# Performance work log

Hardware: AMD Instinct MI355X
Metric: run time of the kernel (lower is better)

Reference implementation:

```python
import jax, jax.numpy as jnp
import numpy as np

B, T, C, H = 2, 2048, 1024, 16
HS = C // H  # head_size = 64
EPS = 1e-5


def _ln(x, g, b):
    m = jnp.mean(x, axis=-1, keepdims=True)
    v = jnp.mean(jnp.square(x - m), axis=-1, keepdims=True)
    return (x - m) * jax.lax.rsqrt(v + EPS) * g + b


def setup_inputs() -> dict:
    key = jax.random.key(0)
    ks = jax.random.split(key, 16)
    s = lambda k, shape, fan: jax.random.normal(k, shape, jnp.float32) * (fan ** -0.5)
    return {
        "x": jax.random.normal(ks[0], (B, T, C), jnp.float32),
        "Wq": s(ks[1], (H, C, HS), C), "bq": jnp.zeros((H, HS), jnp.float32),
        "Wk": s(ks[2], (H, C, HS), C), "bk": jnp.zeros((H, HS), jnp.float32),
        "Wv": s(ks[3], (H, C, HS), C), "bv": jnp.zeros((H, HS), jnp.float32),
        "Wo": s(ks[4], (C, C), C), "bo": jnp.zeros((C,), jnp.float32),
        "g1": jnp.ones((C,), jnp.float32), "b1": jnp.zeros((C,), jnp.float32),
        "g2": jnp.ones((C,), jnp.float32), "b2": jnp.zeros((C,), jnp.float32),
        "W1": s(ks[5], (C, C), C), "bf1": jnp.zeros((C,), jnp.float32),
        "W2": s(ks[6], (C, C), C), "bf2": jnp.zeros((C,), jnp.float32),
    }


def _block(x, Wq, bq, Wk, bk, Wv, bv, Wo, bo, g1, b1, g2, b2, W1, bf1, W2, bf2):
    h = _ln(x, g1, b1)
    # per-head projections, batched over heads: (B,T,C) x (H,C,HS) -> (B,H,T,HS)
    q = jnp.einsum('btc,hcd->bhtd', h, Wq) + bq[None, :, None, :]
    k = jnp.einsum('btc,hcd->bhtd', h, Wk) + bk[None, :, None, :]
    v = jnp.einsum('btc,hcd->bhtd', h, Wv) + bv[None, :, None, :]
    w = jnp.einsum('bhqd,bhkd->bhqk', q, k) * (HS ** -0.5)
    causal = jnp.tril(jnp.ones((T, T), bool))  # tril[q,k]==0 -> -inf
    w = jnp.where(causal[None, None], w, -jnp.inf)
    # FAITHFUL quirk: original uses F.softmax(w, dim=1) on (B,T,T),
    # i.e. normalization over the QUERY axis (axis=2 of bhqk).
    w = jax.nn.softmax(w, axis=2)
    att = jnp.einsum('bhqk,bhkd->bhqd', w, v)
    att = att.transpose(0, 2, 1, 3).reshape(x.shape[0], x.shape[1], -1)  # concat heads
    x = x + att @ Wo + bo
    h2 = _ln(x, g2, b2)
    x = x + jax.nn.relu(h2 @ W1 + bf1) @ W2 + bf2
    return x


def reference(x, Wq, bq, Wk, bk, Wv, bv, Wo, bo, g1, b1, g2, b2, W1, bf1, W2, bf2):
    return _block(x, Wq, bq, Wk, bk, Wv, bv, Wo, bo, g1, b1, g2, b2, W1, bf1, W2, bf2)
```

## Files before the change

### kernel.cpp

```cpp
#include <hip/hip_runtime.h>
#include <hip/hip_bf16.h>
#include <math.h>


#define B_   2
#define T_   2048
#define C_   1024
#define H_   16
#define HS_  64
#define NROWS 4096
#define C3   3072
#define K1C  0.1803368801111244f

typedef unsigned short ushort_t;
typedef __attribute__((ext_vector_type(8))) short short8;
typedef __attribute__((ext_vector_type(4))) float f32x4;
typedef __attribute__((ext_vector_type(16))) float f32x16;

__device__ __forceinline__ ushort_t f2bf(float f) {
  __hip_bfloat16 h = __float2bfloat16(f);
  ushort_t u; __builtin_memcpy(&u, &h, 2); return u;
}
__device__ __forceinline__ float bf2f(ushort_t u) {
  union { unsigned u; float f; } v; v.u = ((unsigned)u) << 16;
  return v.f;
}
__device__ __forceinline__ unsigned pkhw(float a, float b) {
  unsigned u;
  asm("v_cvt_pk_bf16_f32 %0, %1, %2" : "=v"(u) : "v"(a), "v"(b));
  return u;
}
__device__ __forceinline__ short8 mk8(unsigned a, unsigned b, unsigned c, unsigned d) {
  union { unsigned u[4]; short8 s; } t;
  t.u[0] = a; t.u[1] = b; t.u[2] = c; t.u[3] = d; return t.s;
}
__device__ __forceinline__ void pl32swap(unsigned &a, unsigned &b) {
  asm("v_permlane32_swap_b32 %0, %1" : "+v"(a), "+v"(b));
}
__device__ __forceinline__ f32x4 mfma16(short8 a, short8 b, f32x4 c) {
  return __builtin_amdgcn_mfma_f32_16x16x32_bf16(a, b, c, 0, 0, 0);
}
__device__ __forceinline__ f32x16 mfma32(short8 a, short8 b, f32x16 c) {
  return __builtin_amdgcn_mfma_f32_32x32x16_bf16(a, b, c, 0, 0, 0);
}
typedef const __attribute__((address_space(1))) void g_void;
typedef __attribute__((address_space(3))) void l_void;
__device__ __forceinline__ void gl_lds16(const void* g, void* l) {
  __builtin_amdgcn_global_load_lds((g_void*)g, (l_void*)l, 16, 0, 0);
}

__global__ __launch_bounds__(256) void ln_bf16(
    const float* __restrict__ x, const float* __restrict__ g,
    const float* __restrict__ b, ushort_t* __restrict__ out) {
  int row = blockIdx.x;
  const float* xr = x + (size_t)row * C_;
  int t = threadIdx.x;
  float4 v = ((const float4*)xr)[t];
  float s  = v.x + v.y + v.z + v.w;
  float ss = v.x*v.x + v.y*v.y + v.z*v.z + v.w*v.w;
  #pragma unroll
  for (int off = 32; off > 0; off >>= 1) {
    s  += __shfl_down(s, off);
    ss += __shfl_down(ss, off);
  }
  __shared__ float red[2][4];
  int wid = t >> 6, lane = t & 63;
  if (lane == 0) { red[0][wid] = s; red[1][wid] = ss; }
  __syncthreads();
  if (t == 0) {
    float a = 0, c = 0;
    for (int i = 0; i < 4; i++) { a += red[0][i]; c += red[1][i]; }
    red[0][0] = a; red[1][0] = c;
  }
  __syncthreads();
  float mean = red[0][0] * (1.0f / C_);
  float var  = red[1][0] * (1.0f / C_) - mean * mean;
  float r = rsqrtf(var + 1e-5f);
  float4 gv = ((const float4*)g)[t];
  float4 bv = ((const float4*)b)[t];
  ushort4 o;
  o.x = f2bf((v.x - mean) * r * gv.x + bv.x);
  o.y = f2bf((v.y - mean) * r * gv.y + bv.y);
  o.z = f2bf((v.z - mean) * r * gv.z + bv.z);
  o.w = f2bf((v.w - mean) * r * gv.w + bv.w);
  ((ushort4*)(out + (size_t)row * C_))[t] = o;
}

__global__ __launch_bounds__(256) void prep_weights(
    const float* __restrict__ Wq, const float* __restrict__ Wk,
    const float* __restrict__ Wv, const float* __restrict__ Wo,
    const float* __restrict__ W1, const float* __restrict__ W2,
    const float* __restrict__ bq, const float* __restrict__ bk,
    const float* __restrict__ bv, ushort_t* __restrict__ Wqkvt,
    ushort_t* __restrict__ Wot3, float* __restrict__ bqkv) {
  int bid = blockIdx.x;
  if (bid < 12288) {
    int idx = bid * 256 + threadIdx.x;
    int n = idx >> 10, c = idx & 1023;
    int sel = n >> 10, nn = n & 1023;
    const float* W = (sel == 0) ? Wq : ((sel == 1) ? Wk : Wv);
    Wqkvt[idx] = f2bf(W[((size_t)(nn >> 6) * C_ + c) * HS_ + (nn & 63)]);
  } else if (bid < 24576) {
    int idx = (bid - 12288) * 256 + threadIdx.x;
    int sel = idx >> 20, rem = idx & 1048575;
    int n = rem >> 10, k = rem & 1023;
    const float* W = (sel == 0) ? Wo : ((sel == 1) ? W1 : W2);
    Wot3[idx] = f2bf(W[(size_t)k * C_ + n]);
  } else {
    int i = (bid - 24576) * 256 + threadIdx.x;
    if (i < 3072)
      bqkv[i] = (i < 1024) ? bq[i] : ((i < 2048) ? bk[i - 1024] : bv[i - 2048]);
  }
}

__global__ __launch_bounds__(256) void gemm128q(
    const ushort_t* __restrict__ A, const ushort_t* __restrict__ Bt,
    const float* __restrict__ bias, ushort_t* __restrict__ Cm,
    int M, int N, int K) {
  __shared__ ushort_t As[2][128 * 32];
  __shared__ ushort_t Bs[2][128 * 32];
  int t = threadIdx.x;
  int bid = blockIdx.x;
  int xcd = bid & 7, loc = bid >> 3;
  int mb = (xcd >> 1) * 8 + (loc & 7);
  int nb = (xcd & 1) * 12 + (loc >> 3);
  int m0 = mb * 128, n0 = nb * 128;
  int w = t >> 6, l = t & 63;
  int wr = w >> 1, wc = w & 1;
  int lo = l & 15, hi = l >> 4;
  f32x4 acc[4][4] = {};
  int srow = t >> 2;
  int sslot = (t & 3) ^ ((srow >> 1) & 3);
  const ushort_t* Ag = A  + (size_t)(m0 + srow) * K + sslot * 8;
  const ushort_t* Bg = Bt + (size_t)(n0 + srow) * K + sslot * 8;
  int key = (lo >> 1) & 3;
  int aoff[4], boff[4];
  #pragma unroll
  for (int i = 0; i < 4; i++) {
    aoff[i] = (wr * 64 + i * 16 + lo) * 32 + (hi ^ key) * 8;
    boff[i] = (wc * 64 + i * 16 + lo) * 32 + (hi ^ key) * 8;
  }
  int nkt = K >> 5;
  gl_lds16(Ag,          &As[0][t * 8]);
  gl_lds16(Ag + 64 * K, &As[0][64 * 32 + t * 8]);
  gl_lds16(Bg,          &Bs[0][t * 8]);
  gl_lds16(Bg + 64 * K, &Bs[0][64 * 32 + t * 8]);
  for (int kt = 0; kt < nkt; kt++) {
    int cur = kt & 1;
    if (kt + 1 < nkt) {
      int k0 = (kt + 1) * 32;
      gl_lds16(Ag + k0,          &As[cur ^ 1][t * 8]);
      gl_lds16(Ag + 64 * K + k0, &As[cur ^ 1][64 * 32 + t * 8]);
      gl_lds16(Bg + k0,          &Bs[cur ^ 1][t * 8]);
      gl_lds16(Bg + 64 * K + k0, &Bs[cur ^ 1][64 * 32 + t * 8]);
      asm volatile("s_waitcnt vmcnt(4)");
    } else {
      asm volatile("s_waitcnt vmcnt(0)");
    }
    __builtin_amdgcn_s_barrier();
    __builtin_amdgcn_sched_barrier(0);
    short8 af[4], bfr[4];
    #pragma unroll
    for (int i = 0; i < 4; i++) {
      af[i]  = *(const short8*)&As[cur][aoff[i]];
      bfr[i] = *(const short8*)&Bs[cur][boff[i]];
    }
    __builtin_amdgcn_s_setprio(1);
    #pragma unroll
    for (int i = 0; i < 4; i++)
      #pragma unroll
      for (int j = 0; j < 4; j++)
        acc[i][j] = mfma16(af[i], bfr[j], acc[i][j]);
    __builtin_amdgcn_s_setprio(0);
    __builtin_amdgcn_sched_barrier(0);
    __builtin_amdgcn_s_barrier();
    __builtin_amdgcn_sched_barrier(0);
  }
  float qs = (n0 < C_) ? K1C : 1.0f;
  #pragma unroll
  for (int i = 0; i < 4; i++) {
    int m = m0 + wr * 64 + i * 16 + hi * 4;
    #pragma unroll
    for (int j = 0; j < 4; j++) {
      int n = n0 + wc * 64 + j * 16 + lo;
      float bv = bias[n];
      #pragma unroll
      for (int r = 0; r < 4; r++)
        Cm[(size_t)(m + r) * N + n] = f2bf((acc[i][j][r] + bv) * qs);
    }
  }
}

template<int OUT_BF16, int RELU, int HAS_RES>
__global__ __launch_bounds__(256) void gemm64(
    const ushort_t* __restrict__ A, const ushort_t* __restrict__ Bt,
    const float* __restrict__ bias, const float* __restrict__ res,
    void* __restrict__ Cm, int M, int N, int K) {
  __shared__ ushort_t As[2][128 * 32];
  __shared__ ushort_t Bs[2][64 * 32];
  int t = threadIdx.x;
  int m0 = blockIdx.y * 128, n0 = blockIdx.x * 64;
  int w = t >> 6, l = t & 63;
  int wr = w >> 1, wc = w & 1;
  int lo = l & 15, hi = l >> 4;
  f32x4 acc[4][2] = {};
  int srow = t >> 2;
  int sslot = (t & 3) ^ ((srow >> 1) & 3);
  const ushort_t* Ag = A  + (size_t)(m0 + srow) * K + sslot * 8;
  const ushort_t* Bg = Bt + (size_t)(n0 + srow) * K + sslot * 8;
  int key = (lo >> 1) & 3;
  int aoff[4], boff[2];
  #pragma unroll
  for (int i = 0; i < 4; i++)
    aoff[i] = (wr * 64 + i * 16 + lo) * 32 + (hi ^ key) * 8;
  #pragma unroll
  for (int j = 0; j < 2; j++)
    boff[j] = (wc * 32 + j * 16 + lo) * 32 + (hi ^ key) * 8;
  int nkt = K >> 5;
  gl_lds16(Ag,          &As[0][t * 8]);
  gl_lds16(Ag + 64 * K, &As[0][64 * 32 + t * 8]);
  gl_lds16(Bg,          &Bs[0][t * 8]);
  for (int kt = 0; kt < nkt; kt++) {
    int cur = kt & 1;
    if (kt + 1 < nkt) {
      int k0 = (kt + 1) * 32;
      gl_lds16(Ag + k0,          &As[cur ^ 1][t * 8]);
      gl_lds16(Ag + 64 * K + k0, &As[cur ^ 1][64 * 32 + t * 8]);
      gl_lds16(Bg + k0,          &Bs[cur ^ 1][t * 8]);
      asm volatile("s_waitcnt vmcnt(3)");
    } else {
      asm volatile("s_waitcnt vmcnt(0)");
    }
    __builtin_amdgcn_s_barrier();
    __builtin_amdgcn_sched_barrier(0);
    short8 af[4], bfr[2];
    #pragma unroll
    for (int i = 0; i < 4; i++)
      af[i] = *(const short8*)&As[cur][aoff[i]];
    #pragma unroll
    for (int j = 0; j < 2; j++)
      bfr[j] = *(const short8*)&Bs[cur][boff[j]];
    __builtin_amdgcn_s_setprio(1);
    #pragma unroll
    for (int i = 0; i < 4; i++)
      #pragma unroll
      for (int j = 0; j < 2; j++)
        acc[i][j] = mfma16(af[i], bfr[j], acc[i][j]);
    __builtin_amdgcn_s_setprio(0);
    __builtin_amdgcn_sched_barrier(0);
    __builtin_amdgcn_s_barrier();
    __builtin_amdgcn_sched_barrier(0);
  }
  #pragma unroll
  for (int i = 0; i < 4; i++) {
    int m = m0 + wr * 64 + i * 16 + hi * 4;
    #pragma unroll
    for (int j = 0; j < 2; j++) {
      int n = n0 + wc * 32 + j * 16 + lo;
      float bv = bias[n];
      #pragma unroll
      for (int r = 0; r < 4; r++) {
        float v = acc[i][j][r] + bv;
        if (HAS_RES) v += res[(size_t)(m + r) * N + n];
        if (RELU) v = fmaxf(v, 0.f);
        if (OUT_BF16) ((ushort_t*)Cm)[(size_t)(m + r) * N + n] = f2bf(v);
        else          ((float*)Cm)[(size_t)(m + r) * N + n] = v;
      }
    }
  }
}

__global__ __launch_bounds__(256) void attn_stats(
    const ushort_t* __restrict__ QKV, float* __restrict__ dinv) {
  int bid = blockIdx.x;
  int xcd = bid & 7, loc = (bid >> 3) & 31, half = bid >> 8;
  int bh = xcd * 4 + (loc & 3);
  int j = loc >> 2;
  int kb = half ? (15 - j) : j;
  int b = bh >> 4, h = bh & 15;
  int t = threadIdx.x, w = t >> 6, l = t & 63, l31 = l & 31, hi32 = l >> 5;
  __shared__ ushort_t Qs[2][4][2048];
  const ushort_t* Qb = QKV + (size_t)b * T_ * C3 + h * HS_;
  const ushort_t* Kb = Qb + C_;
  int k0w = kb * 128 + w * 32;
  short8 ka[4];
  #pragma unroll
  for (int c = 0; c < 4; c++)
    ka[c] = *(const short8*)(Kb + (size_t)(k0w + l31) * C3 + c * 16 + hi32 * 8);
  float s[16];
  #pragma unroll
  for (int r = 0; r < 16; r++) s[r] = 0.f;

  int qoff[4];
  #pragma unroll
  for (int c = 0; c < 4; c++)
    qoff[c] = l31 * 64 + ((c * 2 + hi32) ^ (l31 & 7)) * 8;

  int sr = t >> 3, slot = t & 7, su = slot ^ (sr & 7);
  const ushort_t* Qsrc = Qb + (size_t)sr * C3 + su * 8;
  int qt0 = kb * 4, cnt = 64 - qt0;
  int dqt = qt0 + w;

  #pragma unroll
  for (int sub = 0; sub < 4; sub++)
    gl_lds16(Qsrc + (size_t)(qt0 + sub) * 32 * C3, &Qs[0][sub][t * 8]);
  for (int i = 0; i < cnt; i += 4) {
    int buf = (i >> 2) & 1;
    if (i + 4 < cnt) {
      #pragma unroll
      for (int sub = 0; sub < 4; sub++)
        gl_lds16(Qsrc + (size_t)(qt0 + i + 4 + sub) * 32 * C3,
                 &Qs[buf ^ 1][sub][t * 8]);
      asm volatile("s_waitcnt vmcnt(4)");
    } else {
      asm volatile("s_waitcnt vmcnt(0)");
    }
    __builtin_amdgcn_s_barrier();
    __builtin_amdgcn_sched_barrier(0);
    #pragma unroll
    for (int sub = 0; sub < 4; sub++) {
      int qt = qt0 + i + sub;
      if (qt >= dqt) {
        const ushort_t* base = &Qs[buf][sub][0];
        short8 qf[4];
        #pragma unroll
        for (int c = 0; c < 4; c++)
          qf[c] = *(const short8*)(base + qoff[c]);
        __builtin_amdgcn_s_setprio(1);
        f32x16 d = {};
        #pragma unroll
        for (int c = 0; c < 4; c++) d = mfma32(ka[c], qf[c], d);
        __builtin_amdgcn_s_setprio(0);
        if (qt == dqt) {
          int qq = qt * 32 + l31;
          #pragma unroll
          for (int r = 0; r < 16; r++) {
            int k = k0w + (r & 3) + 8 * (r >> 2) + 4 * hi32;
            s[r] += (qq >= k) ? __builtin_amdgcn_exp2f(d[r]) : 0.f;
          }
        } else {
          #pragma unroll
          for (int r = 0; r < 16; r++) s[r] += __builtin_amdgcn_exp2f(d[r]);
        }
      }
    }
    __builtin_amdgcn_sched_barrier(0);
    __builtin_amdgcn_s_barrier();
    __builtin_amdgcn_sched_barrier(0);
  }
  #pragma unroll
  for (int off = 1; off < 32; off <<= 1)
    #pragma unroll
    for (int r = 0; r < 16; r++)
      s[r] += __shfl_xor(s[r], off);
  if (l31 == 0) {
    #pragma unroll
    for (int r = 0; r < 16; r++) {
      int k = k0w + (r & 3) + 8 * (r >> 2) + 4 * hi32;
      dinv[(size_t)bh * T_ + k] = 1.0f / s[r];
    }
  }
}

__global__ __launch_bounds__(256) void transpose_v(
    const ushort_t* __restrict__ QKV, const float* __restrict__ dinv,
    ushort_t* __restrict__ Vt) {
  int t0 = blockIdx.x * 64;
  int bh = blockIdx.y; int b = bh >> 4, h = bh & 15;
  __shared__ ushort_t tile[64][65];
  int tid = threadIdx.x;
  #pragma unroll
  for (int i = 0; i < 16; i++) {
    int idx = i * 256 + tid;
    int tt = idx >> 6, dd = idx & 63;
    float v = bf2f(QKV[(size_t)(b * T_ + t0 + tt) * C3 + 2 * C_ + h * HS_ + dd]);
    tile[tt][dd] = f2bf(v * dinv[(size_t)bh * T_ + t0 + tt]);
  }
  __syncthreads();
  #pragma unroll
  for (int i = 0; i < 16; i++) {
    int idx = i * 256 + tid;
    int dd = idx >> 6, tt = idx & 63;
    Vt[((size_t)(bh * HS_ + dd)) * T_ + t0 + tt] = tile[tt][dd];
  }
}

__global__ __launch_bounds__(256) void attn_pv(
    const ushort_t* __restrict__ QKV, const ushort_t* __restrict__ Vt,
    ushort_t* __restrict__ att) {
  int bid = blockIdx.x;
  int xcd = bid & 7, loc = (bid >> 3) & 31, half = bid >> 8;
  int bh = xcd * 4 + (loc & 3);
  int j = loc >> 2;
  int qb = half ? j : (15 - j);
  int b = bh >> 4, h = bh & 15;
  int t = threadIdx.x, w = t >> 6, l = t & 63, l31 = l & 31, hi32 = l >> 5;
  __shared__ ushort_t KV[2][4][2][2048];
  const ushort_t* Qb = QKV + (size_t)b * T_ * C3 + h * HS_;
  const ushort_t* Kb = Qb + C_;
  const ushort_t* Vb = Vt + (size_t)bh * HS_ * T_;
  int q0w = qb * 128 + w * 32;
  short8 qf[4];
  #pragma unroll
  for (int c = 0; c < 4; c++)
    qf[c] = *(const short8*)(Qb + (size_t)(q0w + l31) * C3 + c * 16 + hi32 * 8);
  f32x16 o0 = {}, o1 = {};
  int nkt = qb * 4 + 4;
  int dkt = q0w >> 5;

  int koff[4], voff[4];
  #pragma unroll
  for (int c = 0; c < 4; c++)
    koff[c] = l31 * 64 + ((c * 2 + hi32) ^ (l31 & 7)) * 8;
  #pragma unroll
  for (int i = 0; i < 4; i++) {
    int u = (i & 1) * 4 + (i >> 1) * 2 + hi32;
    voff[i] = 2048 + l31 * 64 + (u ^ (l31 & 7)) * 8;
  }

  int sr = t >> 3, slot = t & 7, su = slot ^ (sr & 7);
  int vdh = su >> 2, vc2 = su & 3;
  const ushort_t* Ksrc = Kb + (size_t)sr * C3 + su * 8;
  const ushort_t* Vsrc = Vb + (size_t)(vdh * 32 + sr) * T_ + vc2 * 8;

  #pragma unroll
  for (int sub = 0; sub < 4; sub++) {
    gl_lds16(Ksrc + (size_t)sub * 32 * C3, &KV[0][sub][0][t * 8]);
    gl_lds16(Vsrc + sub * 32,              &KV[0][sub][1][t * 8]);
  }
  for (int kt = 0; kt < nkt; kt += 4) {
    int buf = (kt >> 2) & 1;
    if (kt + 4 < nkt) {
      #pragma unroll
      for (int sub = 0; sub < 4; sub++) {
        gl_lds16(Ksrc + (size_t)(kt + 4 + sub) * 32 * C3, &KV[buf ^ 1][sub][0][t * 8]);
        gl_lds16(Vsrc + (kt + 4 + sub) * 32,              &KV[buf ^ 1][sub][1][t * 8]);
      }
      asm volatile("s_waitcnt vmcnt(8)");
    } else {
      asm volatile("s_waitcnt vmcnt(0)");
    }
    __builtin_amdgcn_s_barrier();
    __builtin_amdgcn_sched_barrier(0);
    #pragma unroll
    for (int sub = 0; sub < 4; sub++) {
      int kts = kt + sub;
      if (kts <= dkt) {
        const ushort_t* base = &KV[buf][sub][0][0];
        short8 ka[4], vf[4];
        #pragma unroll
        for (int c = 0; c < 4; c++)
          ka[c] = *(const short8*)(base + koff[c]);
        #pragma unroll
        for (int i = 0; i < 4; i++)
          vf[i] = *(const short8*)(base + voff[i]);
        __builtin_amdgcn_s_setprio(1);
        f32x16 sacc = {};
        #pragma unroll
        for (int c = 0; c < 4; c++) sacc = mfma32(ka[c], qf[c], sacc);
        __builtin_amdgcn_s_setprio(0);
        float e[16];
        if (kts == dkt) {
          int qq = q0w + l31;
          #pragma unroll
          for (int r = 0; r < 16; r++) {
            int k = kts * 32 + (r & 3) + 8 * (r >> 2) + 4 * hi32;
            e[r] = (k <= qq) ? __builtin_amdgcn_exp2f(sacc[r]) : 0.f;
          }
        } else {
          #pragma unroll
          for (int r = 0; r < 16; r++) e[r] = __builtin_amdgcn_exp2f(sacc[r]);
        }
        unsigned u[8];
        #pragma unroll
        for (int j2 = 0; j2 < 8; j2++) u[j2] = pkhw(e[2 * j2], e[2 * j2 + 1]);
        pl32swap(u[0], u[2]); pl32swap(u[1], u[3]);
        pl32swap(u[4], u[6]); pl32swap(u[5], u[7]);
        short8 pa0 = mk8(u[0], u[1], u[2], u[3]);
        short8 pa1 = mk8(u[4], u[5], u[6], u[7]);
        __builtin_amdgcn_s_setprio(1);
        o0 = mfma32(pa0, vf[0], o0);
        o1 = mfma32(pa0, vf[1], o1);
        o0 = mfma32(pa1, vf[2], o0);
        o1 = mfma32(pa1, vf[3], o1);
        __builtin_amdgcn_s_setprio(0);
      }
    }
    __builtin_amdgcn_sched_barrier(0);
    __builtin_amdgcn_s_barrier();
    __builtin_amdgcn_sched_barrier(0);
  }

  #pragma unroll
  for (int r = 0; r < 16; r++) {
    int qq = q0w + (r & 3) + 8 * (r >> 2) + 4 * hi32;
    size_t base = (size_t)(b * T_ + qq) * C_ + h * HS_;
    att[base + l31]      = f2bf(o0[r]);
    att[base + 32 + l31] = f2bf(o1[r]);
  }
}

extern "C" void kernel_launch(void* const* d_in, const int* in_sizes, int n_in,
                              void* d_out, int out_size, void* d_ws, size_t ws_size,
                              hipStream_t stream) {
  const float* x   = (const float*)d_in[0];
  const float* Wq  = (const float*)d_in[1];
  const float* bq  = (const float*)d_in[2];
  const float* Wk  = (const float*)d_in[3];
  const float* bk  = (const float*)d_in[4];
  const float* Wv  = (const float*)d_in[5];
  const float* bv  = (const float*)d_in[6];
  const float* Wo  = (const float*)d_in[7];
  const float* bo  = (const float*)d_in[8];
  const float* g1  = (const float*)d_in[9];
  const float* b1  = (const float*)d_in[10];
  const float* g2  = (const float*)d_in[11];
  const float* b2  = (const float*)d_in[12];
  const float* W1  = (const float*)d_in[13];
  const float* bf1 = (const float*)d_in[14];
  const float* W2  = (const float*)d_in[15];
  const float* bf2 = (const float*)d_in[16];
  float* out = (float*)d_out;

  char* base = (char*)d_ws;
  const size_t MB = 1 << 20;
  ushort_t* QKVb  = (ushort_t*)(base);
  ushort_t* hb    = (ushort_t*)(base + 24 * MB);
  ushort_t* Vt    = (ushort_t*)(base + 32 * MB);
  float*    y     = (float*)   (base + 40 * MB);
  ushort_t* Wqkvt = (ushort_t*)(base + 56 * MB);
  ushort_t* Wot   = (ushort_t*)(base + 62 * MB);
  ushort_t* W1t   = (ushort_t*)(base + 64 * MB);
  ushort_t* W2t   = (ushort_t*)(base + 66 * MB);
  float*    bqkv  = (float*)   (base + 68 * MB);
  float*    dinv  = (float*)   (base + 68 * MB + 65536);

  prep_weights<<<24588, 256, 0, stream>>>(Wq, Wk, Wv, Wo, W1, W2,
                                          bq, bk, bv, Wqkvt, Wot, bqkv);

  ln_bf16<<<NROWS, 256, 0, stream>>>(x, g1, b1, hb);

  gemm128q<<<768, 256, 0, stream>>>(hb, Wqkvt, bqkv, QKVb, NROWS, C3, C_);

  attn_stats<<<512, 256, 0, stream>>>(QKVb, dinv);
  transpose_v<<<dim3(T_ / 64, 32), 256, 0, stream>>>(QKVb, dinv, Vt);
  ushort_t* attb = hb;
  attn_pv<<<512, 256, 0, stream>>>(QKVb, Vt, attb);

  dim3 g64(C_ / 64, NROWS / 128);
  gemm64<0,0,1><<<g64, 256, 0, stream>>>(attb, Wot, bo, x, y, NROWS, C_, C_);

  ushort_t* h2b = QKVb;
  ln_bf16<<<NROWS, 256, 0, stream>>>(y, g2, b2, h2b);
  ushort_t* f1b = Vt;
  gemm64<1,1,0><<<g64, 256, 0, stream>>>(h2b, W1t, bf1, nullptr, f1b, NROWS, C_, C_);
  gemm64<0,0,1><<<g64, 256, 0, stream>>>(f1b, W2t, bf2, y, out, NROWS, C_, C_);
}
```

Measured before the change: 202.5 us.

## Tile weight transposes through shared memory and store residual stream in bf16

The weight-prep kernel now transposes 64x64 tiles through padded shared memory, so both the global reads and writes are coalesced, replacing the old per-element strided gathers. The intermediate residual y is now stored in bf16 instead of fp32. A new LayerNorm variant reads bf16 input, and the final GEMM adds a bf16 residual. This cuts memory traffic across three kernels, but rounding the residual stream to bf16 loses precision in the output.

```diff
diff --git a/kernel.cpp b/kernel.cpp
--- a/kernel.cpp
+++ b/kernel.cpp
@@ -86,6 +86,44 @@
   ((ushort4*)(out + (size_t)row * C_))[t] = o;
 }
 
+__global__ __launch_bounds__(256) void ln_bf16_in16(
+    const ushort_t* __restrict__ x, const float* __restrict__ g,
+    const float* __restrict__ b, ushort_t* __restrict__ out) {
+  int row = blockIdx.x;
+  const ushort_t* xr = x + (size_t)row * C_;
+  int t = threadIdx.x;
+  ushort4 uv = ((const ushort4*)xr)[t];
+  float v0 = bf2f(uv.x), v1 = bf2f(uv.y), v2 = bf2f(uv.z), v3 = bf2f(uv.w);
+  float s  = v0 + v1 + v2 + v3;
+  float ss = v0*v0 + v1*v1 + v2*v2 + v3*v3;
+  #pragma unroll
+  for (int off = 32; off > 0; off >>= 1) {
+    s  += __shfl_down(s, off);
+    ss += __shfl_down(ss, off);
+  }
+  __shared__ float red[2][4];
+  int wid = t >> 6, lane = t & 63;
+  if (lane == 0) { red[0][wid] = s; red[1][wid] = ss; }
+  __syncthreads();
+  if (t == 0) {
+    float a = 0, c = 0;
+    for (int i = 0; i < 4; i++) { a += red[0][i]; c += red[1][i]; }
+    red[0][0] = a; red[1][0] = c;
+  }
+  __syncthreads();
+  float mean = red[0][0] * (1.0f / C_);
+  float var  = red[1][0] * (1.0f / C_) - mean * mean;
+  float r = rsqrtf(var + 1e-5f);
+  float4 gv = ((const float4*)g)[t];
+  float4 bv = ((const float4*)b)[t];
+  ushort4 o;
+  o.x = f2bf((v0 - mean) * r * gv.x + bv.x);
+  o.y = f2bf((v1 - mean) * r * gv.y + bv.y);
+  o.z = f2bf((v2 - mean) * r * gv.z + bv.z);
+  o.w = f2bf((v3 - mean) * r * gv.w + bv.w);
+  ((ushort4*)(out + (size_t)row * C_))[t] = o;
+}
+
 __global__ __launch_bounds__(256) void prep_weights(
     const float* __restrict__ Wq, const float* __restrict__ Wk,
     const float* __restrict__ Wv, const float* __restrict__ Wo,
@@ -94,21 +132,49 @@
     const float* __restrict__ bv, ushort_t* __restrict__ Wqkvt,
     ushort_t* __restrict__ Wot3, float* __restrict__ bqkv) {
   int bid = blockIdx.x;
-  if (bid < 12288) {
-    int idx = bid * 256 + threadIdx.x;
-    int n = idx >> 10, c = idx & 1023;
-    int sel = n >> 10, nn = n & 1023;
-    const float* W = (sel == 0) ? Wq : ((sel == 1) ? Wk : Wv);
-    Wqkvt[idx] = f2bf(W[((size_t)(nn >> 6) * C_ + c) * HS_ + (nn & 63)]);
-  } else if (bid < 24576) {
-    int idx = (bid - 12288) * 256 + threadIdx.x;
-    int sel = idx >> 20, rem = idx & 1048575;
-    int n = rem >> 10, k = rem & 1023;
-    const float* W = (sel == 0) ? Wo : ((sel == 1) ? W1 : W2);
-    Wot3[idx] = f2bf(W[(size_t)k * C_ + n]);
+  int tid = threadIdx.x;
+  __shared__ float tile[64][65];
+  if (bid < 768) {
+    int mat = bid >> 8, rem = bid & 255;
+    int h = rem >> 4, ct = rem & 15;
+    const float* W = (mat == 0) ? Wq : ((mat == 1) ? Wk : Wv);
+    const float* src = W + ((size_t)h * C_ + ct * 64) * HS_;
+    #pragma unroll
+    for (int i = 0; i < 16; i++) {
+      int idx = i * 256 + tid;
+      int cc = idx >> 6, dd = idx & 63;
+      tile[cc][dd] = src[(size_t)cc * HS_ + dd];
+    }
+    __syncthreads();
+    #pragma unroll
+    for (int i = 0; i < 16; i++) {
+      int idx = i * 256 + tid;
+      int dd = idx >> 6, cc = idx & 63;
+      Wqkvt[(size_t)(mat * 1024 + h * 64 + dd) * 1024 + ct * 64 + cc] =
+          f2bf(tile[cc][dd]);
+    }
+  } else if (bid < 1536) {
+    int lb = bid - 768;
+    int mat = lb >> 8, rem = lb & 255;
+    int nt = rem >> 4, kt = rem & 15;
+    const float* W = (mat == 0) ? Wo : ((mat == 1) ? W1 : W2);
+    const float* src = W + (size_t)(kt * 64) * C_ + nt * 64;
+    #pragma unroll
+    for (int i = 0; i < 16; i++) {
+      int idx = i * 256 + tid;
+      int kk = idx >> 6, nn = idx & 63;
+      tile[kk][nn] = src[(size_t)kk * C_ + nn];
+    }
+    __syncthreads();
+    #pragma unroll
+    for (int i = 0; i < 16; i++) {
+      int idx = i * 256 + tid;
+      int nn = idx >> 6, kk = idx & 63;
+      Wot3[(size_t)mat * 1048576 + (size_t)(nt * 64 + nn) * 1024 + kt * 64 + kk] =
+          f2bf(tile[kk][nn]);
+    }
   } else {
-    int i = (bid - 24576) * 256 + threadIdx.x;
-    if (i < 3072)
+    for (int i = tid; i < 3072; i += 256)
       bqkv[i] = (i < 1024) ? bq[i] : ((i < 2048) ? bk[i - 1024] : bv[i - 2048]);
   }
 }
@@ -191,10 +257,10 @@
   }
 }
 
-template<int OUT_BF16, int RELU, int HAS_RES>
+template<int OUT_BF16, int RELU, int HAS_RES, int RES_BF16>
 __global__ __launch_bounds__(256) void gemm64(
     const ushort_t* __restrict__ A, const ushort_t* __restrict__ Bt,
-    const float* __restrict__ bias, const float* __restrict__ res,
+    const float* __restrict__ bias, const void* __restrict__ res,
     void* __restrict__ Cm, int M, int N, int K) {
   __shared__ ushort_t As[2][128 * 32];
   __shared__ ushort_t Bs[2][64 * 32];
@@ -261,7 +327,10 @@
       #pragma unroll
       for (int r = 0; r < 4; r++) {
         float v = acc[i][j][r] + bv;
-        if (HAS_RES) v += res[(size_t)(m + r) * N + n];
+        if (HAS_RES) {
+          if (RES_BF16) v += bf2f(((const ushort_t*)res)[(size_t)(m + r) * N + n]);
+          else          v += ((const float*)res)[(size_t)(m + r) * N + n];
+        }
         if (RELU) v = fmaxf(v, 0.f);
         if (OUT_BF16) ((ushort_t*)Cm)[(size_t)(m + r) * N + n] = f2bf(v);
         else          ((float*)Cm)[(size_t)(m + r) * N + n] = v;
@@ -527,7 +596,7 @@
   ushort_t* QKVb  = (ushort_t*)(base);
   ushort_t* hb    = (ushort_t*)(base + 24 * MB);
   ushort_t* Vt    = (ushort_t*)(base + 32 * MB);
-  float*    y     = (float*)   (base + 40 * MB);
+  ushort_t* y     = (ushort_t*)(base + 40 * MB);
   ushort_t* Wqkvt = (ushort_t*)(base + 56 * MB);
   ushort_t* Wot   = (ushort_t*)(base + 62 * MB);
   ushort_t* W1t   = (ushort_t*)(base + 64 * MB);
@@ -535,8 +604,8 @@
   float*    bqkv  = (float*)   (base + 68 * MB);
   float*    dinv  = (float*)   (base + 68 * MB + 65536);
 
-  prep_weights<<<24588, 256, 0, stream>>>(Wq, Wk, Wv, Wo, W1, W2,
-                                          bq, bk, bv, Wqkvt, Wot, bqkv);
+  prep_weights<<<1537, 256, 0, stream>>>(Wq, Wk, Wv, Wo, W1, W2,
+                                         bq, bk, bv, Wqkvt, Wot, bqkv);
 
   ln_bf16<<<NROWS, 256, 0, stream>>>(x, g1, b1, hb);
 
@@ -548,11 +617,11 @@
   attn_pv<<<512, 256, 0, stream>>>(QKVb, Vt, attb);
 
   dim3 g64(C_ / 64, NROWS / 128);
-  gemm64<0,0,1><<<g64, 256, 0, stream>>>(attb, Wot, bo, x, y, NROWS, C_, C_);
+  gemm64<1,0,1,0><<<g64, 256, 0, stream>>>(attb, Wot, bo, x, y, NROWS, C_, C_);
 
   ushort_t* h2b = QKVb;
-  ln_bf16<<<NROWS, 256, 0, stream>>>(y, g2, b2, h2b);
+  ln_bf16_in16<<<NROWS, 256, 0, stream>>>(y, g2, b2, h2b);
   ushort_t* f1b = Vt;
-  gemm64<1,1,0><<<g64, 256, 0, stream>>>(h2b, W1t, bf1, nullptr, f1b, NROWS, C_, C_);
-  gemm64<0,0,1><<<g64, 256, 0, stream>>>(f1b, W2t, bf2, y, out, NROWS, C_, C_);
-}
+  gemm64<1,1,0,0><<<g64, 256, 0, stream>>>(h2b, W1t, bf1, nullptr, f1b, NROWS, C_, C_);
+  gemm64<0,0,1,1><<<g64, 256, 0, stream>>>(f1b, W2t, bf2, y, out, NROWS, C_, C_);
+}
```

Result: faster. 181.7 us (-10.3%).
